# Kernel tuning notes

Hardware: AMD Instinct MI355X
Metric: run time of the kernel (lower is better)

## Reference

```python
import jax, jax.numpy as jnp
import numpy as np

# Module config (mirrors init_kwargs)
VMIN, VMAX = -1.0, 1.0
NUM_ACT_WEIGHTS = 31
INIT_SCALE = 0.04
FEATURES_OUT = 64
N, C, H, W = 8, 64, 256, 256


def setup_inputs() -> dict:
    key = jax.random.key(0)
    x = jax.random.normal(key, (N, C, H, W), dtype=jnp.float32)
    # mu: kernel centers, linspace over [vmin, vmax]
    mu = jnp.asarray(np.linspace(VMIN, VMAX, NUM_ACT_WEIGHTS, dtype=np.float32))
    # sigma: scalar std
    sigma = jnp.float32(2.0 * VMAX / (NUM_ACT_WEIGHTS - 1))
    # w: init_type 'linear' -> init_scale * x_0, repeated over feature channels
    w0 = (INIT_SCALE * np.linspace(VMIN, VMAX, NUM_ACT_WEIGHTS, dtype=np.float32))
    w0 = np.reshape(w0, (1, 1, 1, 1, NUM_ACT_WEIGHTS))
    w = jnp.asarray(np.repeat(w0, FEATURES_OUT, axis=1))  # (1,C,1,1,K)
    return {"x": x, "w": w, "mu": mu, "sigma": sigma}


def reference(x, w, mu, sigma):
    # output = sum_i w[...,i] * exp(-(x - mu_i)^2 / (2 sigma^2))
    inv_two_sig2 = 1.0 / (2.0 * sigma * sigma)
    K = w.shape[-1]
    out = jnp.zeros_like(x)
    # K is small and fixed (31); loop keeps peak memory at one NxCxHxW temp
    for i in range(K):
        d = x - mu[i]
        out = out + w[:, :, :, :, i] * jnp.exp(-(d * d) * inv_two_sig2)
    return out
```

## Files before the change

### kernel.cpp

```cpp
#include <hip/hip_runtime.h>


static constexpr int KW  = 31;
static constexpr int WIN = 7;
static constexpr int RAD = 3;

typedef float f32x4 __attribute__((ext_vector_type(4)));

__device__ __forceinline__ float rbf_one(float xe, const float* __restrict__ wrow,
                                         float mu0, float inv_d, float cd2, float g) {
    const float t = (xe - mu0) * inv_d;
    float jf = rintf(t) - (float)RAD;
    jf = fminf(fmaxf(jf, 0.0f), (float)(KW - WIN));
    const int s = (int)jf;
    float n = t - jf;
    n = fminf(fmaxf(n, -32.0f), 40.0f);
    float E = __builtin_amdgcn_exp2f(cd2 * n * n);
    float r = __builtin_amdgcn_exp2f(cd2 * fmaf(-2.0f, n, 1.0f));
    float acc = 0.0f;
#pragma unroll
    for (int k = 0; k < WIN; ++k) {
        acc = fmaf(wrow[s + k], E, acc);
        E *= r;
        r *= g;
    }
    return acc;
}

__global__ __launch_bounds__(256) void rbf_act_kernel(
    const float* __restrict__ x, const float* __restrict__ w,
    const float* __restrict__ mu, const float* __restrict__ sigma,
    float* __restrict__ out, int n4, int ntot) {
    __shared__ float lw[64 * 32];
    for (int t = threadIdx.x; t < 64 * KW; t += 256) {
        const int ch = t / KW;
        const int i  = t - ch * KW;
        lw[(ch << 5) + i] = w[t];
    }
    __syncthreads();

    const float mu0   = mu[0];
    const float dmu   = (mu[KW - 1] - mu0) * (1.0f / (KW - 1));
    const float inv_d = 1.0f / dmu;
    const float sg    = sigma[0];
    const float cd2   = -1.4426950408889634f * dmu * dmu / (2.0f * sg * sg);
    const float g     = exp2f(2.0f * cd2);

    const int stride = gridDim.x * blockDim.x;
    const int gid    = blockIdx.x * blockDim.x + threadIdx.x;

    for (int i4 = gid; i4 < n4; i4 += stride) {
        const f32x4 xv = reinterpret_cast<const f32x4*>(x)[i4];
        const int c = (i4 >> 14) & 63;
        const float* wrow = &lw[c << 5];

        f32x4 ov;
        ov.x = rbf_one(xv.x, wrow, mu0, inv_d, cd2, g);
        ov.y = rbf_one(xv.y, wrow, mu0, inv_d, cd2, g);
        ov.z = rbf_one(xv.z, wrow, mu0, inv_d, cd2, g);
        ov.w = rbf_one(xv.w, wrow, mu0, inv_d, cd2, g);

        __builtin_nontemporal_store(ov, reinterpret_cast<f32x4*>(out) + i4);
    }

    for (int i = n4 * 4 + gid; i < ntot; i += stride) {
        const int c = (i >> 16) & 63;
        out[i] = rbf_one(x[i], &lw[c << 5], mu0, inv_d, cd2, g);
    }
}

extern "C" void kernel_launch(void* const* d_in, const int* in_sizes, int n_in,
                              void* d_out, int out_size, void* d_ws, size_t ws_size,
                              hipStream_t stream) {
    const float* x  = (const float*)d_in[0];
    const float* w  = (const float*)d_in[1];
    const float* mu = (const float*)d_in[2];
    const float* sg = (const float*)d_in[3];
    float* out = (float*)d_out;

    const int n4 = out_size >> 2;
    int blocks = (n4 + 255) / 256;
    if (blocks > 2048) blocks = 2048;
    if (blocks < 1) blocks = 1;

    rbf_act_kernel<<<blocks, 256, 0, stream>>>(x, w, mu, sg, out, n4, out_size);
}
```

Measured before the change: 48.41 us.

## Replace per-element Gaussian sums with per-block interpolated lookup table

Each block now builds a 1024-entry shared-memory table of the channel's activation over a padded input range, storing value and slope pairs. Each element is then evaluated by linear interpolation instead of a windowed sum of exponentials. The main loop also gets a fixed grid of 4096 blocks with software prefetch of the next input vector. This cuts per-element ALU work at the cost of table construction per block, interpolation error, and a fixed channel-per-block assumption that holds only because the grid stride is a multiple of the channel period.

```diff
diff --git a/kernel.cpp b/kernel.cpp
--- a/kernel.cpp
+++ b/kernel.cpp
@@ -1,13 +1,15 @@
 #include <hip/hip_runtime.h>
 
 
-static constexpr int KW  = 31;
-static constexpr int WIN = 7;
-static constexpr int RAD = 3;
+static constexpr int KW    = 31;
+static constexpr int WIN   = 9;
+static constexpr int RAD   = 4;
+static constexpr int LUT_N = 1024;
 
 typedef float f32x4 __attribute__((ext_vector_type(4)));
+typedef float f32x2 __attribute__((ext_vector_type(2)));
 
-__device__ __forceinline__ float rbf_one(float xe, const float* __restrict__ wrow,
+__device__ __forceinline__ float rbf_win(float xe, const float* __restrict__ wrow,
                                          float mu0, float inv_d, float cd2, float g) {
     const float t = (xe - mu0) * inv_d;
     float jf = rintf(t) - (float)RAD;
@@ -27,45 +29,84 @@
     return acc;
 }
 
-__global__ __launch_bounds__(256) void rbf_act_kernel(
+__global__ __launch_bounds__(256) void rbf_lut_kernel(
     const float* __restrict__ x, const float* __restrict__ w,
     const float* __restrict__ mu, const float* __restrict__ sigma,
-    float* __restrict__ out, int n4, int ntot) {
-    __shared__ float lw[64 * 32];
-    for (int t = threadIdx.x; t < 64 * KW; t += 256) {
-        const int ch = t / KW;
-        const int i  = t - ch * KW;
-        lw[(ch << 5) + i] = w[t];
-    }
-    __syncthreads();
+    float* __restrict__ out, int n4, int ntot, int iters) {
+    __shared__ f32x2 lut2[LUT_N];
+    __shared__ float wrow[32];
+
+    const int tid = threadIdx.x;
+    const int gs  = gridDim.x * blockDim.x;
+    const int gid = blockIdx.x * blockDim.x + tid;
+
+    const int c = (gid >> 14) & 63;
 
     const float mu0   = mu[0];
-    const float dmu   = (mu[KW - 1] - mu0) * (1.0f / (KW - 1));
+    const float muL   = mu[KW - 1];
+    const float dmu   = (muL - mu0) * (1.0f / (KW - 1));
     const float inv_d = 1.0f / dmu;
     const float sg    = sigma[0];
     const float cd2   = -1.4426950408889634f * dmu * dmu / (2.0f * sg * sg);
     const float g     = exp2f(2.0f * cd2);
 
-    const int stride = gridDim.x * blockDim.x;
-    const int gid    = blockIdx.x * blockDim.x + threadIdx.x;
+    const float pad  = 5.25f * sg;
+    const float lo   = mu0 - pad;
+    const float span = (muL - mu0) + 2.0f * pad;
+    const float h    = span * (1.0f / (float)LUT_N);
+    const float invh = (float)LUT_N / span;
+    const float nlo  = -lo * invh;
 
-    for (int i4 = gid; i4 < n4; i4 += stride) {
-        const f32x4 xv = reinterpret_cast<const f32x4*>(x)[i4];
-        const int c = (i4 >> 14) & 63;
-        const float* wrow = &lw[c << 5];
+    int i4 = gid;
+    f32x4 xv = {};
+    if (i4 < n4) xv = reinterpret_cast<const f32x4*>(x)[i4];
 
-        f32x4 ov;
-        ov.x = rbf_one(xv.x, wrow, mu0, inv_d, cd2, g);
-        ov.y = rbf_one(xv.y, wrow, mu0, inv_d, cd2, g);
-        ov.z = rbf_one(xv.z, wrow, mu0, inv_d, cd2, g);
-        ov.w = rbf_one(xv.w, wrow, mu0, inv_d, cd2, g);
+    if (tid < KW) wrow[tid] = w[c * KW + tid];
+    __syncthreads();
 
-        __builtin_nontemporal_store(ov, reinterpret_cast<f32x4*>(out) + i4);
+    for (int e = tid; e < LUT_N; e += 256) {
+        const float xa = lo + (float)e * h;
+        const float a  = rbf_win(xa,     wrow, mu0, inv_d, cd2, g);
+        const float b  = rbf_win(xa + h, wrow, mu0, inv_d, cd2, g);
+        f32x2 p; p.x = a; p.y = b - a;
+        lut2[e] = p;
+    }
+    __syncthreads();
+
+    const float tmax = (float)LUT_N - 0.001f;
+
+    for (int k = 0; k < iters; ++k) {
+        const int next = i4 + gs;
+        f32x4 xn = xv;
+        if (k + 1 < iters && next < n4) xn = reinterpret_cast<const f32x4*>(x)[next];
+
+        if (i4 < n4) {
+            f32x4 ov;
+#pragma unroll
+            for (int e = 0; e < 4; ++e) {
+                float t = fmaf(xv[e], invh, nlo);
+                t = fminf(fmaxf(t, 0.0f), tmax);
+                const int j = (int)t;
+                const float frac = t - (float)j;
+                const f32x2 ab = lut2[j];
+                ov[e] = fmaf(frac, ab.y, ab.x);
+            }
+            __builtin_nontemporal_store(ov, reinterpret_cast<f32x4*>(out) + i4);
+        }
+        xv = xn;
+        i4 = next;
     }
 
-    for (int i = n4 * 4 + gid; i < ntot; i += stride) {
-        const int c = (i >> 16) & 63;
-        out[i] = rbf_one(x[i], &lw[c << 5], mu0, inv_d, cd2, g);
+    const float cd2x = -1.4426950408889634f / (2.0f * sg * sg);
+    for (int i = n4 * 4 + gid; i < ntot; i += gs) {
+        const float xe = x[i];
+        const int ct = (i >> 16) & 63;
+        float acc = 0.0f;
+        for (int q = 0; q < KW; ++q) {
+            const float d = xe - (mu0 + (float)q * dmu);
+            acc = fmaf(w[ct * KW + q], __builtin_amdgcn_exp2f(cd2x * d * d), acc);
+        }
+        out[i] = acc;
     }
 }
 
@@ -78,10 +119,10 @@
     const float* sg = (const float*)d_in[3];
     float* out = (float*)d_out;
 
-    const int n4 = out_size >> 2;
-    int blocks = (n4 + 255) / 256;
-    if (blocks > 2048) blocks = 2048;
-    if (blocks < 1) blocks = 1;
+    const int n4     = out_size >> 2;
+    const int blocks = 4096;
+    const int gsz    = blocks * 256;
+    const int iters  = (n4 + gsz - 1) / gsz;
 
-    rbf_act_kernel<<<blocks, 256, 0, stream>>>(x, w, mu, sg, out, n4, out_size);
+    rbf_lut_kernel<<<blocks, 256, 0, stream>>>(x, w, mu, sg, out, n4, out_size, iters);
 }
```

Measured after the change: 44.95 us. -7.1%, faster.
